# Optimization experiments

Hardware: AMD Instinct MI355X
Metric: run time of the kernel (lower is better)

The kernel has to match this reference:

```python
import jax, jax.numpy as jnp
import numpy as np

ZERO_EXP = -128.0  # exponent assigned to (near-)zero values, matching torch int8 fill


def _exp_quant_dequant(t):
    """Round-trip through the ExpFloat format.

    exponent = clamp(round(log2(|t|)), -128, 127) for |t| > 1e-38 else -128.
    Dequant is pow(2, exponent) -- note the sign is DISCARDED (faithful to
    ExpFloat.to_tensor, which never applies the stored sign), so the result
    is always positive.
    """
    a = jnp.abs(t)
    mask = a > 1e-38
    # guard log2 input with 1.0 where masked to avoid -inf/nan
    e = jnp.clip(jnp.round(jnp.log2(jnp.where(mask, a, 1.0))), -128.0, 127.0)
    e = jnp.where(mask, e, ZERO_EXP)
    return jnp.exp2(e)


def setup_inputs() -> dict:
    key = jax.random.key(0)
    k1, k2, k3 = jax.random.split(key, 3)
    N, IN, OUT = 8192, 4096, 4096
    x = jax.random.normal(k1, (N, IN), dtype=jnp.float32)
    # kaiming-uniform-ish scale for weight, uniform bias bound 1/sqrt(fan_in)
    bound_w = float(np.sqrt(6.0 / ((1.0 + 5.0) * IN)))
    weight = jax.random.uniform(k2, (OUT, IN), dtype=jnp.float32,
                                minval=-bound_w, maxval=bound_w)
    bound_b = 1.0 / float(np.sqrt(IN))
    bias = jax.random.uniform(k3, (OUT,), dtype=jnp.float32,
                              minval=-bound_b, maxval=bound_b)
    return {"x": x, "weight": weight, "bias": bias}


def reference(x, weight, bias):
    # quantized forward path of ExpFloatLinear (after .quantize()):
    # 1) x and W.T are quantized to power-of-two magnitudes (sign dropped)
    xq = _exp_quant_dequant(x)             # [N, IN]
    wq = _exp_quant_dequant(weight.T)      # [IN, OUT]
    # 2) dense matmul in dequantized domain
    m = jnp.matmul(xq, wq)                 # [N, OUT]
    # 3) matmul result re-quantized (ExpFloat.matmul returns ExpFloat(result))
    mq = _exp_quant_dequant(m)
    # 4) bias dequantized, added, and the sum quantized once more before to_tensor
    bq = _exp_quant_dequant(bias)          # [OUT]
    out = _exp_quant_dequant(mq + bq)      # [N, OUT]
    return out
```

## Files before the change

kernel.cpp:

```cpp
#include <hip/hip_runtime.h>
#include <hip/hip_bf16.h>
#include <stdint.h>

typedef __attribute__((ext_vector_type(8))) short short8;
typedef __attribute__((ext_vector_type(4))) float f32x4;

#define M_ROWS 8192
#define K_DIM  4096
#define N_COLS 4096
#define NT     (K_DIM / 64)
#define WL_CAP (1 << 20)

#define SQRT2_MANT 0x6A09E667F3BCDLL
#define FLAG_MARGIN 3110000000000LL

__device__ __forceinline__ int rlog2_mask(double a) {
    if (!(a > 1e-38)) return -128;
    long long b = __double_as_longlong(a);
    int E = (int)(b >> 52) - 1023;
    long long m = b & 0xFFFFFFFFFFFFFLL;
    int e = E + (int)(m >= SQRT2_MANT);
    return e < -128 ? -128 : (e > 127 ? 127 : e);
}

__device__ __forceinline__ double pow2d(int e) {
    return __longlong_as_double((long long)(e + 1023) << 52);
}

__device__ __forceinline__ unsigned short bf16_pow2(int e) {
    if (e >= -126) return (unsigned short)((e + 127) << 7);
    int sh = 133 + e;
    return (unsigned short)(sh >= 0 ? (1 << sh) : 0);
}

__device__ __forceinline__ int bf16_exp(unsigned short u) {
    int ex = (u >> 7) & 0xFF;
    if (ex) return ex - 127;
    int m = u & 0x7F;
    return m ? (-133 + (31 - __clz(m))) : -1000;
}

__device__ __forceinline__ float finalize_out(int em, int ebj) {
    double s = pow2d(em) + pow2d(ebj);
    return (float)pow2d(rlog2_mask(s));
}

__device__ __forceinline__ ushort4 quant4(float4 v) {
    ushort4 o;
    o.x = bf16_pow2(rlog2_mask(fabs((double)v.x)));
    o.y = bf16_pow2(rlog2_mask(fabs((double)v.y)));
    o.z = bf16_pow2(rlog2_mask(fabs((double)v.z)));
    o.w = bf16_pow2(rlog2_mask(fabs((double)v.w)));
    return o;
}

__global__ void quant_kernel(const float* __restrict__ x, const float* __restrict__ w,
                             unsigned short* __restrict__ xq, unsigned short* __restrict__ wq,
                             int nx4, int nw4) {
    int idx = blockIdx.x * blockDim.x + threadIdx.x;
    int stride = gridDim.x * blockDim.x;
    int total = nx4 + nw4;
    for (int i = idx; i < total; i += stride) {
        if (i < nx4) {
            float4 v = ((const float4*)x)[i];
            ((ushort4*)xq)[i] = quant4(v);
        } else {
            float4 v = ((const float4*)w)[i - nx4];
            ((ushort4*)wq)[i - nx4] = quant4(v);
        }
    }
}

__global__ void quant_bias_kernel(const float* __restrict__ b, int* __restrict__ eb, int n) {
    int i = blockIdx.x * blockDim.x + threadIdx.x;
    if (i < n) eb[i] = rlog2_mask(fabs((double)b[i]));
}

__device__ __forceinline__ void g2lds16(const unsigned short* g, unsigned short* l) {
    __builtin_amdgcn_global_load_lds(
        (const __attribute__((address_space(1))) unsigned int*)g,
        (__attribute__((address_space(3))) unsigned int*)l, 16, 0, 0);
}

#define LD8(p, off) (*(const short8*)((const char*)(p) + (off)))
#define MFMA16(a, b, c) __builtin_amdgcn_mfma_f32_16x16x32_bf16((a), (b), (c), 0, 0, 0)

__global__ __launch_bounds__(512, 2) void gemm_kernel(
    const unsigned short* __restrict__ xq, const unsigned short* __restrict__ wq,
    const int* __restrict__ eb, float* __restrict__ out,
    int* __restrict__ wl_count, int* __restrict__ wl)
{
    __shared__ unsigned short lds[2][32768];

    const int tid = threadIdx.x;
    const int lane = tid & 63, w = tid >> 6;
    const int wm = w >> 2, wn = w & 3;
    const int l15 = lane & 15, lhi = lane >> 4;

    const int x = blockIdx.x & 7;
    const int j = blockIdx.x >> 3;
    const int bm0 = (x & 3) * 8 + (j & 3);
    const int bn  = (x >> 2) * 8 + (j >> 2);
    const int bcol = bn * 256;

    int p0 = tid * 16;
    int lin0 = p0 ^ (((p0 >> 9) & 1) << 5);
    int row0 = (lin0 >> 6) & 127;
    int col0 = (((lin0 >> 13) << 6) | (lin0 & 63)) >> 1;
    int p1 = 8192 + tid * 16;
    int lin1 = p1 ^ (((p1 >> 9) & 1) << 5);
    int row1 = (lin1 >> 6) & 127;
    int col1 = (((lin1 >> 13) << 6) | (lin1 & 63)) >> 1;

    int fsw = l15 * 64 + lhi * 16;
    fsw ^= ((l15 >> 3) & 1) << 5;

    const char* pA_0 = (const char*)&lds[0][wm * 8192] + fsw;
    const char* pA_1 = (const char*)&lds[1][wm * 8192] + fsw;
    const char* pB_0 = (const char*)&lds[0][16384 + (wn >> 1) * 8192 + (wn & 1) * 2048] + fsw;
    const char* pB_1 = (const char*)&lds[1][16384 + (wn >> 1) * 8192 + (wn & 1) * 2048] + fsw;

#define STAGE_A(b, h, OFFE) do { \
        g2lds16(((h) ? aS0h1 : aS0h0) + (OFFE), &lds[b][(h) * 8192] + wofs); \
        g2lds16(((h) ? aS1h1 : aS1h0) + (OFFE), &lds[b][(h) * 8192 + 4096] + wofs); \
    } while (0)
#define STAGE_B(b, h, OFFE) do { \
        g2lds16(((h) ? bS0h1 : bS0h0) + (OFFE), &lds[b][16384 + (h) * 8192] + wofs); \
        g2lds16(((h) ? bS1h1 : bS1h0) + (OFFE), &lds[b][16384 + (h) * 8192 + 4096] + wofs); \
    } while (0)
#define DS_A4(P, mb) do { \
        aF[0][0] = LD8(P, ((mb) + 0) * 1024); aF[0][1] = LD8(P, ((mb) + 0) * 1024 + 8192); \
        aF[1][0] = LD8(P, ((mb) + 1) * 1024); aF[1][1] = LD8(P, ((mb) + 1) * 1024 + 8192); \
        aF[2][0] = LD8(P, ((mb) + 2) * 1024); aF[2][1] = LD8(P, ((mb) + 2) * 1024 + 8192); \
        aF[3][0] = LD8(P, ((mb) + 3) * 1024); aF[3][1] = LD8(P, ((mb) + 3) * 1024 + 8192); \
    } while (0)
#define DS_B2(P, arr, cb) do { \
        arr[0][0] = LD8(P, ((cb) + 0) * 1024); arr[0][1] = LD8(P, ((cb) + 0) * 1024 + 8192); \
        arr[1][0] = LD8(P, ((cb) + 1) * 1024); arr[1][1] = LD8(P, ((cb) + 1) * 1024 + 8192); \
    } while (0)
#define MFMA_Q(mb, nb, B) do { \
        _Pragma("unroll") \
        for (int m_ = 0; m_ < 4; ++m_) \
        _Pragma("unroll") \
        for (int n_ = 0; n_ < 2; ++n_) { \
            acc[(mb) + m_][(nb) + n_] = MFMA16(aF[m_][0], B[n_][0], acc[(mb) + m_][(nb) + n_]); \
            acc[(mb) + m_][(nb) + n_] = MFMA16(aF[m_][1], B[n_][1], acc[(mb) + m_][(nb) + n_]); \
        } \
    } while (0)

#define BAR()  __builtin_amdgcn_s_barrier()
#define PRIO1() __builtin_amdgcn_s_setprio(1)
#define PRIO0() __builtin_amdgcn_s_setprio(0)

    const int wofs = w * 512;

    for (int ht = 0; ht < 2; ++ht) {
        const int bm = bm0 + ht * 4;
        const int brow = bm * 256;

        const unsigned short* aS0h0 = xq + (size_t)(brow + row0) * K_DIM + col0;
        const unsigned short* aS1h0 = xq + (size_t)(brow + row1) * K_DIM + col1;
        const unsigned short* aS0h1 = aS0h0 + (size_t)128 * K_DIM;
        const unsigned short* aS1h1 = aS1h0 + (size_t)128 * K_DIM;
        const unsigned short* bS0h0 = wq + (size_t)(bcol + row0) * K_DIM + col0;
        const unsigned short* bS1h0 = wq + (size_t)(bcol + row1) * K_DIM + col1;
        const unsigned short* bS0h1 = bS0h0 + (size_t)128 * K_DIM;
        const unsigned short* bS1h1 = bS1h0 + (size_t)128 * K_DIM;

        f32x4 acc[8][4];
#pragma unroll
        for (int m = 0; m < 8; ++m)
#pragma unroll
            for (int n = 0; n < 4; ++n) acc[m][n] = (f32x4){0.f, 0.f, 0.f, 0.f};

        short8 aF[4][2], b01[2][2], b23[2][2];

        STAGE_A(0, 0, 0);
        STAGE_A(0, 1, 0);
        STAGE_B(0, 0, 0);
        STAGE_B(0, 1, 0);
        STAGE_B(1, 0, 64);
        STAGE_B(1, 1, 64);
        asm volatile("s_waitcnt vmcnt(4)" ::: "memory");
        BAR();

        for (int tt = 0; tt < NT / 2 - 1; ++tt) {
            DS_B2(pB_0, b01, 0); DS_B2(pB_0, b23, 2);
            DS_A4(pA_0, 0);
            STAGE_A(1, 0, 64); STAGE_A(1, 1, 64);
            PRIO1(); MFMA_Q(0, 0, b01); MFMA_Q(0, 2, b23); PRIO0(); BAR();
            DS_A4(pA_0, 4);
            STAGE_B(0, 0, 128); STAGE_B(0, 1, 128);
            PRIO1(); MFMA_Q(4, 2, b23); MFMA_Q(4, 0, b01); PRIO0();
            asm volatile("s_waitcnt vmcnt(4)" ::: "memory");
            BAR();
            DS_B2(pB_1, b01, 0); DS_B2(pB_1, b23, 2);
            DS_A4(pA_1, 0);
            STAGE_A(0, 0, 128); STAGE_A(0, 1, 128);
            PRIO1(); MFMA_Q(0, 0, b01); MFMA_Q(0, 2, b23); PRIO0(); BAR();
            DS_A4(pA_1, 4);
            STAGE_B(1, 0, 192); STAGE_B(1, 1, 192);
            PRIO1(); MFMA_Q(4, 2, b23); MFMA_Q(4, 0, b01); PRIO0();
            asm volatile("s_waitcnt vmcnt(4)" ::: "memory");
            BAR();

            aS0h0 += 128; aS1h0 += 128; aS0h1 += 128; aS1h1 += 128;
            bS0h0 += 128; bS1h0 += 128; bS0h1 += 128; bS1h1 += 128;
        }

        DS_B2(pB_0, b01, 0); DS_B2(pB_0, b23, 2);
        DS_A4(pA_0, 0);
        STAGE_A(1, 0, 64); STAGE_A(1, 1, 64);
        PRIO1(); MFMA_Q(0, 0, b01); MFMA_Q(0, 2, b23); PRIO0(); BAR();
        DS_A4(pA_0, 4);
        PRIO1(); MFMA_Q(4, 2, b23); MFMA_Q(4, 0, b01); PRIO0();
        asm volatile("s_waitcnt vmcnt(0)" ::: "memory");
        BAR();
        DS_B2(pB_1, b01, 0); DS_B2(pB_1, b23, 2);
        DS_A4(pA_1, 0);
        PRIO1(); MFMA_Q(0, 0, b01); MFMA_Q(0, 2, b23); PRIO0(); BAR();
        DS_A4(pA_1, 4);
        PRIO1(); MFMA_Q(4, 2, b23); MFMA_Q(4, 0, b01); PRIO0();

        BAR();

#pragma unroll
        for (int m = 0; m < 8; ++m) {
            int grow_base = brow + wm * 128 + m * 16 + lhi * 4;
#pragma unroll
            for (int n = 0; n < 4; ++n) {
                int gcol = bcol + wn * 64 + n * 16 + l15;
                int ebj = eb[gcol];
#pragma unroll
                for (int q = 0; q < 4; ++q) {
                    float S = acc[m][n][q];
                    int grow = grow_base + q;
                    double v = (double)S;
                    int em; bool flag;
                    if (v > 1e-38) {
                        long long bb = __double_as_longlong(v);
                        long long mm = bb & 0xFFFFFFFFFFFFFLL;
                        long long d = mm - SQRT2_MANT;
                        flag = (d < 0 ? -d : d) < FLAG_MARGIN;
                        int e = ((int)(bb >> 52) - 1023) + (int)(mm >= SQRT2_MANT);
                        em = e < -128 ? -128 : (e > 127 ? 127 : e);
                    } else { em = -128; flag = true; }
                    out[(size_t)grow * N_COLS + gcol] = finalize_out(em, ebj);
                    if (flag) {
                        int pos = atomicAdd(wl_count, 1);
                        if (pos < WL_CAP) wl[pos] = grow * N_COLS + gcol;
                    }
                }
            }
        }
    }
}

__global__ __launch_bounds__(256) void fixup_kernel(
    const unsigned short* __restrict__ xq, const unsigned short* __restrict__ wq,
    const int* __restrict__ eb, float* __restrict__ out,
    const int* __restrict__ wl_count, const int* __restrict__ wl)
{
    const int nwaves = (gridDim.x * blockDim.x) >> 6;
    const int gw = (blockIdx.x * blockDim.x + threadIdx.x) >> 6;
    const int lane = threadIdx.x & 63;
    int count = *wl_count;
    if (count > WL_CAP) count = WL_CAP;
    for (int it = gw; it < count; it += nwaves) {
        int lin = wl[it];
        int i = lin >> 12;
        int j = lin & 4095;
        const unsigned short* xr = xq + (size_t)i * K_DIM;
        const unsigned short* wr = wq + (size_t)j * K_DIM;
        unsigned long long accu = 0;
        for (int kb = 0; kb < K_DIM / 256; ++kb) {
            int k0 = kb * 256 + lane * 4;
            ushort4 xv = *(const ushort4*)(xr + k0);
            ushort4 wv = *(const ushort4*)(wr + k0);
            int p;
            p = bf16_exp(xv.x) + bf16_exp(wv.x) + 56; if ((unsigned)p <= 62u) accu += 1ULL << p;
            p = bf16_exp(xv.y) + bf16_exp(wv.y) + 56; if ((unsigned)p <= 62u) accu += 1ULL << p;
            p = bf16_exp(xv.z) + bf16_exp(wv.z) + 56; if ((unsigned)p <= 62u) accu += 1ULL << p;
            p = bf16_exp(xv.w) + bf16_exp(wv.w) + 56; if ((unsigned)p <= 62u) accu += 1ULL << p;
        }
#pragma unroll
        for (int off = 32; off; off >>= 1) accu += __shfl_down(accu, off, 64);
        if (lane == 0) {
            double S = (double)accu * 0x1p-56;
            int em = rlog2_mask(S);
            out[lin] = finalize_out(em, eb[j]);
        }
    }
}

extern "C" void kernel_launch(void* const* d_in, const int* in_sizes, int n_in,
                              void* d_out, int out_size, void* d_ws, size_t ws_size,
                              hipStream_t stream) {
    const float* x    = (const float*)d_in[0];
    const float* w    = (const float*)d_in[1];
    const float* bias = (const float*)d_in[2];
    float* out = (float*)d_out;
    char* ws = (char*)d_ws;

    int* wl_count = (int*)ws;
    int* eb       = (int*)(ws + 256);
    unsigned short* xq = (unsigned short*)(ws + 32768);
    unsigned short* wq = (unsigned short*)(ws + 32768 + (size_t)M_ROWS * K_DIM * 2);
    int* wl = (int*)(ws + 32768 + (size_t)M_ROWS * K_DIM * 2 + (size_t)N_COLS * K_DIM * 2);

    hipMemsetAsync(wl_count, 0, 4, stream);
    quant_kernel<<<3072, 256, 0, stream>>>(x, w, xq, wq,
                                           M_ROWS * K_DIM / 4, N_COLS * K_DIM / 4);
    quant_bias_kernel<<<16, 256, 0, stream>>>(bias, eb, N_COLS);
    gemm_kernel<<<dim3(256), 512, 0, stream>>>(xq, wq, eb, out, wl_count, wl);
    fixup_kernel<<<1024, 256, 0, stream>>>(xq, wq, eb, out, wl_count, wl);
}
```

Baseline: 278.4 us.

## Double-buffer A fragments in registers to overlap LDS reads with MFMA

Splits the A-fragment registers into two sets so the next half-tile's A fragments are read from LDS while MFMAs on the current set run. This removes one LDS-read-then-compute serialization per half step. It merges the post-wait barrier into the MFMA phase. It raises register pressure, and it reads the other LDS buffer after only a per-wave vmcnt wait rather than a workgroup barrier, which may race with other waves' async loads.

```diff
diff --git a/kernel.cpp b/kernel.cpp
--- a/kernel.cpp
+++ b/kernel.cpp
@@ -128,23 +128,23 @@
         g2lds16(((h) ? bS0h1 : bS0h0) + (OFFE), &lds[b][16384 + (h) * 8192] + wofs); \
         g2lds16(((h) ? bS1h1 : bS1h0) + (OFFE), &lds[b][16384 + (h) * 8192 + 4096] + wofs); \
     } while (0)
-#define DS_A4(P, mb) do { \
-        aF[0][0] = LD8(P, ((mb) + 0) * 1024); aF[0][1] = LD8(P, ((mb) + 0) * 1024 + 8192); \
-        aF[1][0] = LD8(P, ((mb) + 1) * 1024); aF[1][1] = LD8(P, ((mb) + 1) * 1024 + 8192); \
-        aF[2][0] = LD8(P, ((mb) + 2) * 1024); aF[2][1] = LD8(P, ((mb) + 2) * 1024 + 8192); \
-        aF[3][0] = LD8(P, ((mb) + 3) * 1024); aF[3][1] = LD8(P, ((mb) + 3) * 1024 + 8192); \
+#define DS_A4(DST, P, mb) do { \
+        DST[0][0] = LD8(P, ((mb) + 0) * 1024); DST[0][1] = LD8(P, ((mb) + 0) * 1024 + 8192); \
+        DST[1][0] = LD8(P, ((mb) + 1) * 1024); DST[1][1] = LD8(P, ((mb) + 1) * 1024 + 8192); \
+        DST[2][0] = LD8(P, ((mb) + 2) * 1024); DST[2][1] = LD8(P, ((mb) + 2) * 1024 + 8192); \
+        DST[3][0] = LD8(P, ((mb) + 3) * 1024); DST[3][1] = LD8(P, ((mb) + 3) * 1024 + 8192); \
     } while (0)
 #define DS_B2(P, arr, cb) do { \
         arr[0][0] = LD8(P, ((cb) + 0) * 1024); arr[0][1] = LD8(P, ((cb) + 0) * 1024 + 8192); \
         arr[1][0] = LD8(P, ((cb) + 1) * 1024); arr[1][1] = LD8(P, ((cb) + 1) * 1024 + 8192); \
     } while (0)
-#define MFMA_Q(mb, nb, B) do { \
+#define MFMA_Q(A, mb, nb, B) do { \
         _Pragma("unroll") \
         for (int m_ = 0; m_ < 4; ++m_) \
         _Pragma("unroll") \
         for (int n_ = 0; n_ < 2; ++n_) { \
-            acc[(mb) + m_][(nb) + n_] = MFMA16(aF[m_][0], B[n_][0], acc[(mb) + m_][(nb) + n_]); \
-            acc[(mb) + m_][(nb) + n_] = MFMA16(aF[m_][1], B[n_][1], acc[(mb) + m_][(nb) + n_]); \
+            acc[(mb) + m_][(nb) + n_] = MFMA16(A[m_][0], B[n_][0], acc[(mb) + m_][(nb) + n_]); \
+            acc[(mb) + m_][(nb) + n_] = MFMA16(A[m_][1], B[n_][1], acc[(mb) + m_][(nb) + n_]); \
         } \
     } while (0)
 
@@ -173,7 +173,7 @@
 #pragma unroll
             for (int n = 0; n < 4; ++n) acc[m][n] = (f32x4){0.f, 0.f, 0.f, 0.f};
 
-        short8 aF[4][2], b01[2][2], b23[2][2];
+        short8 aA[4][2], aB[4][2], b01[2][2], b23[2][2];
 
         STAGE_A(0, 0, 0);
         STAGE_A(0, 1, 0);
@@ -182,45 +182,42 @@
         STAGE_B(1, 0, 64);
         STAGE_B(1, 1, 64);
         asm volatile("s_waitcnt vmcnt(4)" ::: "memory");
+        DS_A4(aA, pA_0, 0);
         BAR();
 
         for (int tt = 0; tt < NT / 2 - 1; ++tt) {
             DS_B2(pB_0, b01, 0); DS_B2(pB_0, b23, 2);
-            DS_A4(pA_0, 0);
+            DS_A4(aB, pA_0, 4);
             STAGE_A(1, 0, 64); STAGE_A(1, 1, 64);
-            PRIO1(); MFMA_Q(0, 0, b01); MFMA_Q(0, 2, b23); PRIO0(); BAR();
-            DS_A4(pA_0, 4);
+            PRIO1(); MFMA_Q(aA, 0, 0, b01); MFMA_Q(aA, 0, 2, b23); PRIO0(); BAR();
             STAGE_B(0, 0, 128); STAGE_B(0, 1, 128);
-            PRIO1(); MFMA_Q(4, 2, b23); MFMA_Q(4, 0, b01); PRIO0();
             asm volatile("s_waitcnt vmcnt(4)" ::: "memory");
-            BAR();
+            DS_A4(aA, pA_1, 0);
+            PRIO1(); MFMA_Q(aB, 4, 0, b01); MFMA_Q(aB, 4, 2, b23); PRIO0(); BAR();
             DS_B2(pB_1, b01, 0); DS_B2(pB_1, b23, 2);
-            DS_A4(pA_1, 0);
+            DS_A4(aB, pA_1, 4);
             STAGE_A(0, 0, 128); STAGE_A(0, 1, 128);
-            PRIO1(); MFMA_Q(0, 0, b01); MFMA_Q(0, 2, b23); PRIO0(); BAR();
-            DS_A4(pA_1, 4);
+            PRIO1(); MFMA_Q(aA, 0, 0, b01); MFMA_Q(aA, 0, 2, b23); PRIO0(); BAR();
             STAGE_B(1, 0, 192); STAGE_B(1, 1, 192);
-            PRIO1(); MFMA_Q(4, 2, b23); MFMA_Q(4, 0, b01); PRIO0();
             asm volatile("s_waitcnt vmcnt(4)" ::: "memory");
-            BAR();
+            DS_A4(aA, pA_0, 0);
+            PRIO1(); MFMA_Q(aB, 4, 0, b01); MFMA_Q(aB, 4, 2, b23); PRIO0(); BAR();
 
             aS0h0 += 128; aS1h0 += 128; aS0h1 += 128; aS1h1 += 128;
             bS0h0 += 128; bS1h0 += 128; bS0h1 += 128; bS1h1 += 128;
         }
 
         DS_B2(pB_0, b01, 0); DS_B2(pB_0, b23, 2);
-        DS_A4(pA_0, 0);
+        DS_A4(aB, pA_0, 4);
         STAGE_A(1, 0, 64); STAGE_A(1, 1, 64);
-        PRIO1(); MFMA_Q(0, 0, b01); MFMA_Q(0, 2, b23); PRIO0(); BAR();
-        DS_A4(pA_0, 4);
-        PRIO1(); MFMA_Q(4, 2, b23); MFMA_Q(4, 0, b01); PRIO0();
+        PRIO1(); MFMA_Q(aA, 0, 0, b01); MFMA_Q(aA, 0, 2, b23); PRIO0(); BAR();
         asm volatile("s_waitcnt vmcnt(0)" ::: "memory");
-        BAR();
+        DS_A4(aA, pA_1, 0);
+        PRIO1(); MFMA_Q(aB, 4, 0, b01); MFMA_Q(aB, 4, 2, b23); PRIO0(); BAR();
         DS_B2(pB_1, b01, 0); DS_B2(pB_1, b23, 2);
-        DS_A4(pA_1, 0);
-        PRIO1(); MFMA_Q(0, 0, b01); MFMA_Q(0, 2, b23); PRIO0(); BAR();
-        DS_A4(pA_1, 4);
-        PRIO1(); MFMA_Q(4, 2, b23); MFMA_Q(4, 0, b01); PRIO0();
+        DS_A4(aB, pA_1, 4);
+        PRIO1(); MFMA_Q(aA, 0, 0, b01); MFMA_Q(aA, 0, 2, b23); PRIO0(); BAR();
+        PRIO1(); MFMA_Q(aB, 4, 0, b01); MFMA_Q(aB, 4, 2, b23); PRIO0();
 
         BAR();
 
```

New measurement: 408.2 us. 1.47x slower.

## Shrink GEMM block tile to 128x256 with K-step 32 and 4 waves

Applied to the files above, without the earlier changes.

Restructures the GEMM from 512-thread blocks computing 256x256 tiles with K-chunks of 64 into 256-thread blocks computing 128x256 tiles with K-chunks of 32. The grid doubles to 512 blocks, LDS per block drops from 128KB to 48KB, and the staging and fragment-load patterns are rewritten to match. The goal is better occupancy and CU load balance. The cost is less operand reuse per block, more global and L2 traffic, and twice as many barriers per unit of K.

```diff
diff --git a/kernel.cpp b/kernel.cpp
--- a/kernel.cpp
+++ b/kernel.cpp
@@ -8,7 +8,7 @@
 #define M_ROWS 8192
 #define K_DIM  4096
 #define N_COLS 4096
-#define NT     (K_DIM / 64)
+#define NT     (K_DIM / 32)
 #define WL_CAP (1 << 20)
 
 #define SQRT2_MANT 0x6A09E667F3BCDLL
@@ -85,67 +85,64 @@
 #define LD8(p, off) (*(const short8*)((const char*)(p) + (off)))
 #define MFMA16(a, b, c) __builtin_amdgcn_mfma_f32_16x16x32_bf16((a), (b), (c), 0, 0, 0)
 
-__global__ __launch_bounds__(512, 2) void gemm_kernel(
+__global__ __launch_bounds__(256, 2) void gemm_kernel(
     const unsigned short* __restrict__ xq, const unsigned short* __restrict__ wq,
     const int* __restrict__ eb, float* __restrict__ out,
     int* __restrict__ wl_count, int* __restrict__ wl)
 {
-    __shared__ unsigned short lds[2][32768];
+    __shared__ unsigned short lds[2][12288];
 
     const int tid = threadIdx.x;
     const int lane = tid & 63, w = tid >> 6;
-    const int wm = w >> 2, wn = w & 3;
+    const int wn = w;
     const int l15 = lane & 15, lhi = lane >> 4;
 
     const int x = blockIdx.x & 7;
     const int j = blockIdx.x >> 3;
-    const int bm0 = (x & 3) * 8 + (j & 3);
-    const int bn  = (x >> 2) * 8 + (j >> 2);
+    const int bn  = x * 2 + (j >> 5);
+    const int bm0 = (j & 31) * 2;
     const int bcol = bn * 256;
 
-    int p0 = tid * 16;
-    int lin0 = p0 ^ (((p0 >> 9) & 1) << 5);
-    int row0 = (lin0 >> 6) & 127;
-    int col0 = (((lin0 >> 13) << 6) | (lin0 & 63)) >> 1;
-    int p1 = 8192 + tid * 16;
-    int lin1 = p1 ^ (((p1 >> 9) & 1) << 5);
-    int row1 = (lin1 >> 6) & 127;
-    int col1 = (((lin1 >> 13) << 6) | (lin1 & 63)) >> 1;
+    const int rs = tid >> 2;
+    const int colb = (((tid & 3) * 16)) ^ (((tid >> 5) & 1) << 5);
+    const int col_e = colb >> 1;
 
     int fsw = l15 * 64 + lhi * 16;
     fsw ^= ((l15 >> 3) & 1) << 5;
 
-    const char* pA_0 = (const char*)&lds[0][wm * 8192] + fsw;
-    const char* pA_1 = (const char*)&lds[1][wm * 8192] + fsw;
-    const char* pB_0 = (const char*)&lds[0][16384 + (wn >> 1) * 8192 + (wn & 1) * 2048] + fsw;
-    const char* pB_1 = (const char*)&lds[1][16384 + (wn >> 1) * 8192 + (wn & 1) * 2048] + fsw;
-
-#define STAGE_A(b, h, OFFE) do { \
-        g2lds16(((h) ? aS0h1 : aS0h0) + (OFFE), &lds[b][(h) * 8192] + wofs); \
-        g2lds16(((h) ? aS1h1 : aS1h0) + (OFFE), &lds[b][(h) * 8192 + 4096] + wofs); \
-    } while (0)
-#define STAGE_B(b, h, OFFE) do { \
-        g2lds16(((h) ? bS0h1 : bS0h0) + (OFFE), &lds[b][16384 + (h) * 8192] + wofs); \
-        g2lds16(((h) ? bS1h1 : bS1h0) + (OFFE), &lds[b][16384 + (h) * 8192 + 4096] + wofs); \
+    const char* pA_0 = (const char*)&lds[0][0] + fsw;
+    const char* pA_1 = (const char*)&lds[1][0] + fsw;
+    const char* pB_0 = (const char*)&lds[0][0] + 8192 + wn * 4096 + fsw;
+    const char* pB_1 = (const char*)&lds[1][0] + 8192 + wn * 4096 + fsw;
+
+#define STAGE_A(b, OFFE) do { \
+        g2lds16(aS0 + (OFFE), &lds[b][0]    + wofs); \
+        g2lds16(aS1 + (OFFE), &lds[b][2048] + wofs); \
+    } while (0)
+#define STAGE_B(b, OFFE) do { \
+        g2lds16(bS0 + (OFFE), &lds[b][4096]  + wofs); \
+        g2lds16(bS1 + (OFFE), &lds[b][6144]  + wofs); \
+        g2lds16(bS2 + (OFFE), &lds[b][8192]  + wofs); \
+        g2lds16(bS3 + (OFFE), &lds[b][10240] + wofs); \
     } while (0)
 #define DS_A4(P, mb) do { \
-        aF[0][0] = LD8(P, ((mb) + 0) * 1024); aF[0][1] = LD8(P, ((mb) + 0) * 1024 + 8192); \
-        aF[1][0] = LD8(P, ((mb) + 1) * 1024); aF[1][1] = LD8(P, ((mb) + 1) * 1024 + 8192); \
-        aF[2][0] = LD8(P, ((mb) + 2) * 1024); aF[2][1] = LD8(P, ((mb) + 2) * 1024 + 8192); \
-        aF[3][0] = LD8(P, ((mb) + 3) * 1024); aF[3][1] = LD8(P, ((mb) + 3) * 1024 + 8192); \
-    } while (0)
-#define DS_B2(P, arr, cb) do { \
-        arr[0][0] = LD8(P, ((cb) + 0) * 1024); arr[0][1] = LD8(P, ((cb) + 0) * 1024 + 8192); \
-        arr[1][0] = LD8(P, ((cb) + 1) * 1024); arr[1][1] = LD8(P, ((cb) + 1) * 1024 + 8192); \
-    } while (0)
-#define MFMA_Q(mb, nb, B) do { \
+        aF[0] = LD8(P, ((mb) + 0) * 1024); \
+        aF[1] = LD8(P, ((mb) + 1) * 1024); \
+        aF[2] = LD8(P, ((mb) + 2) * 1024); \
+        aF[3] = LD8(P, ((mb) + 3) * 1024); \
+    } while (0)
+#define DS_B4(P) do { \
+        bF[0] = LD8(P, 0 * 1024); \
+        bF[1] = LD8(P, 1 * 1024); \
+        bF[2] = LD8(P, 2 * 1024); \
+        bF[3] = LD8(P, 3 * 1024); \
+    } while (0)
+#define MFMA_G(mb) do { \
         _Pragma("unroll") \
         for (int m_ = 0; m_ < 4; ++m_) \
         _Pragma("unroll") \
-        for (int n_ = 0; n_ < 2; ++n_) { \
-            acc[(mb) + m_][(nb) + n_] = MFMA16(aF[m_][0], B[n_][0], acc[(mb) + m_][(nb) + n_]); \
-            acc[(mb) + m_][(nb) + n_] = MFMA16(aF[m_][1], B[n_][1], acc[(mb) + m_][(nb) + n_]); \
-        } \
+        for (int n_ = 0; n_ < 4; ++n_) \
+            acc[(mb) + m_][n_] = MFMA16(aF[m_], bF[n_], acc[(mb) + m_][n_]); \
     } while (0)
 
 #define BAR()  __builtin_amdgcn_s_barrier()
@@ -155,17 +152,15 @@
     const int wofs = w * 512;
 
     for (int ht = 0; ht < 2; ++ht) {
-        const int bm = bm0 + ht * 4;
-        const int brow = bm * 256;
-
-        const unsigned short* aS0h0 = xq + (size_t)(brow + row0) * K_DIM + col0;
-        const unsigned short* aS1h0 = xq + (size_t)(brow + row1) * K_DIM + col1;
-        const unsigned short* aS0h1 = aS0h0 + (size_t)128 * K_DIM;
-        const unsigned short* aS1h1 = aS1h0 + (size_t)128 * K_DIM;
-        const unsigned short* bS0h0 = wq + (size_t)(bcol + row0) * K_DIM + col0;
-        const unsigned short* bS1h0 = wq + (size_t)(bcol + row1) * K_DIM + col1;
-        const unsigned short* bS0h1 = bS0h0 + (size_t)128 * K_DIM;
-        const unsigned short* bS1h1 = bS1h0 + (size_t)128 * K_DIM;
+        const int bm = bm0 + ht;
+        const int brow = bm * 128;
+
+        const unsigned short* aS0 = xq + (size_t)(brow +   0 + rs) * K_DIM + col_e;
+        const unsigned short* aS1 = xq + (size_t)(brow +  64 + rs) * K_DIM + col_e;
+        const unsigned short* bS0 = wq + (size_t)(bcol +   0 + rs) * K_DIM + col_e;
+        const unsigned short* bS1 = wq + (size_t)(bcol +  64 + rs) * K_DIM + col_e;
+        const unsigned short* bS2 = wq + (size_t)(bcol + 128 + rs) * K_DIM + col_e;
+        const unsigned short* bS3 = wq + (size_t)(bcol + 192 + rs) * K_DIM + col_e;
 
         f32x4 acc[8][4];
 #pragma unroll
@@ -173,60 +168,56 @@
 #pragma unroll
             for (int n = 0; n < 4; ++n) acc[m][n] = (f32x4){0.f, 0.f, 0.f, 0.f};
 
-        short8 aF[4][2], b01[2][2], b23[2][2];
-
-        STAGE_A(0, 0, 0);
-        STAGE_A(0, 1, 0);
-        STAGE_B(0, 0, 0);
-        STAGE_B(0, 1, 0);
-        STAGE_B(1, 0, 64);
-        STAGE_B(1, 1, 64);
+        short8 aF[4], bF[4];
+
+        STAGE_A(0, 0);
+        STAGE_B(0, 0);
+        STAGE_B(1, 32);
         asm volatile("s_waitcnt vmcnt(4)" ::: "memory");
         BAR();
 
         for (int tt = 0; tt < NT / 2 - 1; ++tt) {
-            DS_B2(pB_0, b01, 0); DS_B2(pB_0, b23, 2);
+            DS_B4(pB_0);
             DS_A4(pA_0, 0);
-            STAGE_A(1, 0, 64); STAGE_A(1, 1, 64);
-            PRIO1(); MFMA_Q(0, 0, b01); MFMA_Q(0, 2, b23); PRIO0(); BAR();
+            STAGE_A(1, 32);
+            PRIO1(); MFMA_G(0); PRIO0(); BAR();
             DS_A4(pA_0, 4);
-            STAGE_B(0, 0, 128); STAGE_B(0, 1, 128);
-            PRIO1(); MFMA_Q(4, 2, b23); MFMA_Q(4, 0, b01); PRIO0();
+            STAGE_B(0, 64);
+            PRIO1(); MFMA_G(4); PRIO0();
             asm volatile("s_waitcnt vmcnt(4)" ::: "memory");
             BAR();
-            DS_B2(pB_1, b01, 0); DS_B2(pB_1, b23, 2);
+            DS_B4(pB_1);
             DS_A4(pA_1, 0);
-            STAGE_A(0, 0, 128); STAGE_A(0, 1, 128);
-            PRIO1(); MFMA_Q(0, 0, b01); MFMA_Q(0, 2, b23); PRIO0(); BAR();
+            STAGE_A(0, 64);
+            PRIO1(); MFMA_G(0); PRIO0(); BAR();
             DS_A4(pA_1, 4);
-            STAGE_B(1, 0, 192); STAGE_B(1, 1, 192);
-            PRIO1(); MFMA_Q(4, 2, b23); MFMA_Q(4, 0, b01); PRIO0();
+            STAGE_B(1, 96);
+            PRIO1(); MFMA_G(4); PRIO0();
             asm volatile("s_waitcnt vmcnt(4)" ::: "memory");
             BAR();
 
-            aS0h0 += 128; aS1h0 += 128; aS0h1 += 128; aS1h1 += 128;
-            bS0h0 += 128; bS1h0 += 128; bS0h1 += 128; bS1h1 += 128;
-        }
-
-        DS_B2(pB_0, b01, 0); DS_B2(pB_0, b23, 2);
+            aS0 += 64; aS1 += 64; bS0 += 64; bS1 += 64; bS2 += 64; bS3 += 64;
+        }
+
+        DS_B4(pB_0);
         DS_A4(pA_0, 0);
-        STAGE_A(1, 0, 64); STAGE_A(1, 1, 64);
-        PRIO1(); MFMA_Q(0, 0, b01); MFMA_Q(0, 2, b23); PRIO0(); BAR();
+        STAGE_A(1, 32);
+        PRIO1(); MFMA_G(0); PRIO0(); BAR();
         DS_A4(pA_0, 4);
-        PRIO1(); MFMA_Q(4, 2, b23); MFMA_Q(4, 0, b01); PRIO0();
+        PRIO1(); MFMA_G(4); PRIO0();
         asm volatile("s_waitcnt vmcnt(0)" ::: "memory");
         BAR();
-        DS_B2(pB_1, b01, 0); DS_B2(pB_1, b23, 2);
+        DS_B4(pB_1);
         DS_A4(pA_1, 0);
-        PRIO1(); MFMA_Q(0, 0, b01); MFMA_Q(0, 2, b23); PRIO0(); BAR();
+        PRIO1(); MFMA_G(0); PRIO0(); BAR();
         DS_A4(pA_1, 4);
-        PRIO1(); MFMA_Q(4, 2, b23); MFMA_Q(4, 0, b01); PRIO0();
+        PRIO1(); MFMA_G(4); PRIO0();
 
         BAR();
 
 #pragma unroll
         for (int m = 0; m < 8; ++m) {
-            int grow_base = brow + wm * 128 + m * 16 + lhi * 4;
+            int grow_base = brow + m * 16 + lhi * 4;
 #pragma unroll
             for (int n = 0; n < 4; ++n) {
                 int gcol = bcol + wn * 64 + n * 16 + l15;
@@ -312,6 +303,6 @@
     quant_kernel<<<3072, 256, 0, stream>>>(x, w, xq, wq,
                                            M_ROWS * K_DIM / 4, N_COLS * K_DIM / 4);
     quant_bias_kernel<<<16, 256, 0, stream>>>(bias, eb, N_COLS);
-    gemm_kernel<<<dim3(256), 512, 0, stream>>>(xq, wq, eb, out, wl_count, wl);
+    gemm_kernel<<<dim3(512), 256, 0, stream>>>(xq, wq, eb, out, wl_count, wl);
     fixup_kernel<<<1024, 256, 0, stream>>>(xq, wq, eb, out, wl_count, wl);
 }
```

Result: slower. 408.3 us (+46.7%).
